# Kernel optimization log

Measured on AMD Instinct MI355X. Metric: run time of the kernel, lower is better.

## Reference

```python
import jax, jax.numpy as jnp
import numpy as np
from jax import lax

B, S, D, H = 64, 256, 512, 8
DH = D // H
FILTER_HEIGHTS = (1, 3, 5)


def setup_inputs() -> dict:
    key = jax.random.key(0)
    ks = jax.random.split(key, 20)
    w = lambda k, shape, s=0.02: (jax.random.normal(k, shape, dtype=jnp.float32) * s)
    inp = {
        "x": jax.random.normal(ks[0], (B, S, D), dtype=jnp.float32),
        "particles": jax.random.uniform(ks[1], (B, S, 3), dtype=jnp.float32),
        # QKV and output projections
        "wq": w(ks[2], (D, D)),
        "wk": w(ks[3], (D, D)),
        "wv": w(ks[4], (D, D)),
        "dense_w": w(ks[5], (D, D)),
        "dense_b": jnp.zeros((D,), jnp.float32),
        # attention-score smoothing convs: kernel (h, S, 1, 1) HWIO, full-width
        "conv1_k": w(ks[6], (1, S, 1, 1)),
        "conv1_b": jnp.zeros((1,), jnp.float32),
        "conv3_k": w(ks[7], (3, S, 1, 1)),
        "conv3_b": jnp.zeros((1,), jnp.float32),
        "conv5_k": w(ks[8], (5, S, 1, 1)),
        "conv5_b": jnp.zeros((1,), jnp.float32),
        # pairwise-feature mask net (1x1 convs == per-pair MLP): 4->8->8->1
        "mw1": w(ks[9], (4, 8), 0.1),
        "mb1": jnp.zeros((8,), jnp.float32),
        "mw2": w(ks[10], (8, 8), 0.1),
        "mb2": jnp.zeros((8,), jnp.float32),
        "mw3": w(ks[11], (8, 1), 0.1),
        "mb3": jnp.zeros((1,), jnp.float32),
    }
    return inp


def _conv_same(x, kern, bias):
    # x: [N, S, S, 1], kern: [h, S, 1, 1] -> [N, S, S, 1], TF 'same' padding, stride 1
    y = lax.conv_general_dilated(x, kern, window_strides=(1, 1), padding="SAME",
                                 dimension_numbers=("NHWC", "HWIO", "NHWC"))
    return y + bias


def _pairwise_features(particles):
    pt, eta, phi = particles[..., 0], particles[..., 1], particles[..., 2]
    pt_i, pt_j = pt[:, :, None], pt[:, None, :]
    d_eta = eta[:, :, None] - eta[:, None, :]
    dp = phi[:, :, None] - phi[:, None, :]
    d_phi = jnp.arctan2(jnp.sin(dp), jnp.cos(dp))
    delta = jnp.sqrt(d_eta ** 2 + d_phi ** 2)
    min_pt = jnp.minimum(pt_i, pt_j)
    kT = min_pt * delta
    z = min_pt / (pt_i + pt_j + 1e-8)
    m2 = jnp.maximum(pt_i ** 2 + pt_j ** 2 - 2.0 * pt_i * pt_j * jnp.cos(d_phi), 1e-8)
    eps = 1e-8
    return jnp.stack([
        jnp.log(jnp.maximum(delta, eps)),
        jnp.log(jnp.maximum(kT, eps)),
        jnp.log(jnp.maximum(z, eps)),
        jnp.log(m2),
    ], axis=-1)  # [B, S, S, 4]


def reference(x, particles, wq, wk, wv, dense_w, dense_b,
              conv1_k, conv1_b, conv3_k, conv3_b, conv5_k, conv5_b,
              mw1, mb1, mw2, mb2, mw3, mb3):
    b = x.shape[0]
    split = lambda t: t.reshape(b, S, H, DH).transpose(0, 2, 1, 3)  # [B,H,S,DH]
    q, k, v = split(x @ wq), split(x @ wk), split(x @ wv)

    scores = jnp.einsum("bhqd,bhkd->bhqk", q, k) / jnp.sqrt(jnp.float32(DH))

    # conv smoothing over score matrices (avg of full-width convs h in {1,3,5})
    xs = scores.reshape(b * H, S, S, 1)
    c1 = _conv_same(xs, conv1_k, conv1_b)
    c3 = _conv_same(xs, conv3_k, conv3_b)
    c5 = _conv_same(xs, conv5_k, conv5_b)
    scores = ((c1 + c3 + c5) / 3.0).reshape(b, H, S, S)

    # pairwise-feature mask (1x1 conv net == per-pair MLP)
    feats = _pairwise_features(particles)               # [B,S,S,4]
    m = jax.nn.relu(feats @ mw1 + mb1)
    m = jax.nn.relu(m @ mw2 + mb2)
    m = (m @ mw3 + mb3)[..., 0]                         # [B,S,S]
    m = jnp.clip(m, -10.0, 10.0)
    scores = scores + m[:, None, :, :]

    weights = jax.nn.softmax(scores, axis=-1)
    attn = jnp.einsum("bhqk,bhkd->bhqd", weights, v)
    concat = attn.transpose(0, 2, 1, 3).reshape(b, S, D)
    return concat @ dense_w + dense_b
```

## Files before the change

kernel.cpp:

```cpp
#include <hip/hip_runtime.h>
#include <hip/hip_bf16.h>
#include <math.h>

#define B   64
#define S   256
#define DD  512
#define H   8
#define DH  64
#define BH  (B*H)

typedef short s16x8 __attribute__((ext_vector_type(8)));
typedef short s16x4 __attribute__((ext_vector_type(4)));
typedef float f32x4 __attribute__((ext_vector_type(4)));

typedef __attribute__((address_space(3))) unsigned int       lds_u32;
typedef __attribute__((address_space(1))) const unsigned int glb_u32;

__device__ __forceinline__ short f2bf(float f) {
    union { float f; unsigned u; } v; v.f = f;
    unsigned u = v.u;
    u += 0x7FFFu + ((u >> 16) & 1u);
    return (short)(u >> 16);
}

__device__ __forceinline__ void glds16(const void* g, void* l) {
    __builtin_amdgcn_global_load_lds((glb_u32*)g, (lds_u32*)l, 16, 0, 0);
}

__global__ __launch_bounds__(256) void convert_x_kernel(
    const float* __restrict__ x, ushort* __restrict__ xbf)
{
    const int idx = blockIdx.x * 256 + threadIdx.x;
    const float4 f0 = *(const float4*)(x + (size_t)idx * 8);
    const float4 f1 = *(const float4*)(x + (size_t)idx * 8 + 4);
    s16x8 o = { f2bf(f0.x), f2bf(f0.y), f2bf(f0.z), f2bf(f0.w),
                f2bf(f1.x), f2bf(f1.y), f2bf(f1.z), f2bf(f1.w) };
    *(s16x8*)(xbf + (size_t)idx * 8) = o;
}

__global__ __launch_bounds__(256) void transpose_w_kernel(
    const float* __restrict__ wq, const float* __restrict__ wk,
    const float* __restrict__ wv, const float* __restrict__ wd,
    ushort* __restrict__ wt)
{
    __shared__ float tile[32][33];
    const int z = blockIdx.z;
    const float* w = (z == 0) ? wq : (z == 1) ? wk : (z == 2) ? wv : wd;
    const int k0 = blockIdx.y * 32, n0 = blockIdx.x * 32;
    const int tx = threadIdx.x & 31, ty = threadIdx.x >> 5;

    #pragma unroll
    for (int r = 0; r < 32; r += 8)
        tile[ty + r][tx] = w[(size_t)(k0 + ty + r) * DD + n0 + tx];
    __syncthreads();
    #pragma unroll
    for (int r = 0; r < 32; r += 8)
        wt[(size_t)z * DD * DD + (size_t)(n0 + ty + r) * DD + k0 + tx] =
            (ushort)f2bf(tile[tx][ty + r]);
}

__global__ __launch_bounds__(256) void build_toeplitz_frag_kernel(
    const float* __restrict__ c1k, const float* __restrict__ c3k,
    const float* __restrict__ c5k, ushort* __restrict__ btf)
{
    const int idx  = blockIdx.x * 256 + threadIdx.x;
    const int lane = idx & 63;
    const int st   = (idx >> 6) % 40;
    const int n    = idx / (40 * 64);
    const int c    = n * 16 + (lane & 15);
    const int r    = st >> 3;
    const int tb   = (st & 7) * 32 + (lane >> 4) * 8;

    s16x8 o;
    #pragma unroll
    for (int e = 0; e < 8; ++e) {
        const int ki = tb + e - c + 127;
        float val = 0.f;
        if (ki >= 0 && ki < 256) {
            val = c5k[r * 256 + ki];
            if (r >= 1 && r <= 3) val += c3k[(r - 1) * 256 + ki];
            if (r == 2)           val += c1k[ki];
            val *= (1.f / 24.f);
        }
        o[e] = f2bf(val);
    }
    *(s16x8*)(btf + (size_t)idx * 8) = o;
}

__global__ __launch_bounds__(256) void vfrag_repack_kernel(
    const ushort* __restrict__ vbT, ushort* __restrict__ vfrag)
{
    const int idx  = blockIdx.x * 256 + threadIdx.x;
    const int lane = idx & 63;
    const int kk   = (idx >> 6) & 7;
    const int n    = (idx >> 9) & 3;
    const int head = idx >> 11;
    const s16x8 v = *(const s16x8*)(vbT
        + ((size_t)(head * 64 + n * 16 + (lane & 15))) * 256
        + kk * 32 + (lane >> 4) * 8);
    *(s16x8*)(vfrag + (size_t)idx * 8) = v;
}

template<int MODE>
__global__ __launch_bounds__(256) void gemm_mfma_kernel(
    const ushort* __restrict__ A, const ushort* __restrict__ BtAll,
    ushort* __restrict__ qo, ushort* __restrict__ ko, ushort* __restrict__ vo,
    const float* __restrict__ bias, float* __restrict__ outf)
{
    __shared__ ushort As[128 * 64];
    __shared__ ushort Bs[128 * 64];

    const int tid  = threadIdx.x;
    const int lane = tid & 63, w = tid >> 6;
    const int l15  = lane & 15, l4 = lane >> 4;
    const int wr   = w >> 1, wc = w & 1;
    const int row0 = blockIdx.y * 128, col0 = blockIdx.x * 128;
    const ushort* Bt = BtAll + (MODE == 0 ? (size_t)blockIdx.z * DD * DD : 0);

    f32x4 acc[4][4];
    #pragma unroll
    for (int mt = 0; mt < 4; ++mt)
        #pragma unroll
        for (int nt = 0; nt < 4; ++nt)
            acc[mt][nt] = (f32x4){0.f, 0.f, 0.f, 0.f};

    const int arow = tid >> 3;
    const int acol = (tid & 7) * 8;
    char* ldsA = (char*)As + (tid >> 6) * 1024;
    char* ldsB = (char*)Bs + (tid >> 6) * 1024;

    for (int k0 = 0; k0 < DD; k0 += 64) {
        #pragma unroll
        for (int i = 0; i < 4; ++i)
            glds16(A  + (size_t)(row0 + arow + 32 * i) * DD + k0 + acol,
                   ldsA + 4096 * i);
        #pragma unroll
        for (int i = 0; i < 4; ++i)
            glds16(Bt + (size_t)(col0 + arow + 32 * i) * DD + k0 + acol,
                   ldsB + 4096 * i);
        __syncthreads();

        #pragma unroll
        for (int kk = 0; kk < 2; ++kk) {
            s16x8 af[4], bf[4];
            #pragma unroll
            for (int mt = 0; mt < 4; ++mt) {
                const int row = wr * 64 + mt * 16 + l15;
                af[mt] = *(const s16x8*)((char*)As + row * 128 + kk * 64 + l4 * 16);
            }
            #pragma unroll
            for (int nt = 0; nt < 4; ++nt) {
                const int col = wc * 64 + nt * 16 + l15;
                bf[nt] = *(const s16x8*)((char*)Bs + col * 128 + kk * 64 + l4 * 16);
            }
            #pragma unroll
            for (int mt = 0; mt < 4; ++mt)
                #pragma unroll
                for (int nt = 0; nt < 4; ++nt)
                    acc[mt][nt] = __builtin_amdgcn_mfma_f32_16x16x32_bf16(
                                      af[mt], bf[nt], acc[mt][nt], 0, 0, 0);
        }
        __syncthreads();
    }

    if (MODE == 0) {
        if (blockIdx.z == 2) {
            #pragma unroll
            for (int mt = 0; mt < 4; ++mt)
                #pragma unroll
                for (int nt = 0; nt < 4; ++nt) {
                    const int r = row0 + wr * 64 + mt * 16 + l4 * 4;
                    const int c = col0 + wc * 64 + nt * 16 + l15;
                    const int bb = r >> 8, ss = r & 255;
                    const int hh = c >> 6, dd = c & 63;
                    s16x4 pk = { f2bf(acc[mt][nt][0]), f2bf(acc[mt][nt][1]),
                                 f2bf(acc[mt][nt][2]), f2bf(acc[mt][nt][3]) };
                    *(s16x4*)(vo + ((size_t)((bb * H + hh) * DH + dd)) * S + ss) = pk;
                }
        } else {
            ushort* dst = (blockIdx.z == 0) ? qo : ko;
            #pragma unroll
            for (int mt = 0; mt < 4; ++mt)
                #pragma unroll
                for (int nt = 0; nt < 4; ++nt)
                    #pragma unroll
                    for (int rg = 0; rg < 4; ++rg) {
                        const int r = row0 + wr * 64 + mt * 16 + l4 * 4 + rg;
                        const int c = col0 + wc * 64 + nt * 16 + l15;
                        const int bb = r >> 8, ss = r & 255;
                        const int hh = c >> 6, dd = c & 63;
                        dst[(((size_t)(bb * H + hh)) * S + ss) * DH + dd] =
                            (ushort)f2bf(acc[mt][nt][rg]);
                    }
        }
    } else {
        #pragma unroll
        for (int mt = 0; mt < 4; ++mt)
            #pragma unroll
            for (int nt = 0; nt < 4; ++nt)
                #pragma unroll
                for (int rg = 0; rg < 4; ++rg) {
                    const int r = row0 + wr * 64 + mt * 16 + l4 * 4 + rg;
                    const int c = col0 + wc * 64 + nt * 16 + l15;
                    outf[(size_t)r * DD + c] = acc[mt][nt][rg] + bias[c];
                }
    }
}

__global__ __launch_bounds__(256) void pairwise_mlp_kernel(
    const float* __restrict__ particles,
    const float* __restrict__ mw1, const float* __restrict__ mb1,
    const float* __restrict__ mw2, const float* __restrict__ mb2,
    const float* __restrict__ mw3, const float* __restrict__ mb3,
    const float* __restrict__ c1b, const float* __restrict__ c3b,
    const float* __restrict__ c5b,
    float* __restrict__ mfrag)
{
    __shared__ float w1[32], b1[8], w2[64], b2[8], w3[8];
    __shared__ float b3s;
    const int tid = threadIdx.x;
    if (tid < 32)                 w1[tid]        = mw1[tid];
    if (tid >= 32 && tid < 40)    b1[tid - 32]   = mb1[tid - 32];
    if (tid >= 64 && tid < 128)   w2[tid - 64]   = mw2[tid - 64];
    if (tid >= 128 && tid < 136)  b2[tid - 128]  = mb2[tid - 128];
    if (tid >= 136 && tid < 144)  w3[tid - 136]  = mw3[tid - 136];
    if (tid == 144)               b3s            = mb3[0];

    const int bi = blockIdx.x;
    const int bb = bi >> 8;
    const float pt_i  = particles[(size_t)bi * 3 + 0];
    const float eta_i = particles[(size_t)bi * 3 + 1];
    const float phi_i = particles[(size_t)bi * 3 + 2];

    const int j = tid;
    const float* pj = particles + ((size_t)(bb * S) + j) * 3;
    const float pt_j = pj[0], eta_j = pj[1], phi_j = pj[2];

    __syncthreads();

    const float d_eta = eta_i - eta_j;
    const float dp    = phi_i - phi_j;
    const float d_phi = atan2f(sinf(dp), cosf(dp));
    const float delta = sqrtf(d_eta * d_eta + d_phi * d_phi);
    const float min_pt = fminf(pt_i, pt_j);
    const float kT = min_pt * delta;
    const float zf = min_pt / (pt_i + pt_j + 1e-8f);
    const float cd = cosf(d_phi);
    const float m2 = fmaxf(pt_i * pt_i + pt_j * pt_j - 2.0f * pt_i * pt_j * cd, 1e-8f);

    const float eps = 1e-8f;
    const float f[4] = { logf(fmaxf(delta, eps)),
                         logf(fmaxf(kT,    eps)),
                         logf(fmaxf(zf,    eps)),
                         logf(m2) };

    float h1[8];
    #pragma unroll
    for (int o = 0; o < 8; ++o) {
        float s = b1[o];
        #pragma unroll
        for (int i4 = 0; i4 < 4; ++i4) s += f[i4] * w1[i4 * 8 + o];
        h1[o] = fmaxf(s, 0.0f);
    }
    float h2[8];
    #pragma unroll
    for (int o = 0; o < 8; ++o) {
        float s = b2[o];
        #pragma unroll
        for (int i8 = 0; i8 < 8; ++i8) s += h1[i8] * w2[i8 * 8 + o];
        h2[o] = fmaxf(s, 0.0f);
    }
    float mv = b3s;
    #pragma unroll
    for (int i8 = 0; i8 < 8; ++i8) mv += h2[i8] * w3[i8];
    mv = fminf(fmaxf(mv, -10.0f), 10.0f);
    mv += (c1b[0] + c3b[0] + c5b[0]) * (1.f / 3.f);

    const int ii     = bi & 255;
    const int chunk2 = ii >> 7;
    const int rem    = ii & 127;
    const int wr     = rem >> 6, rt = (rem >> 4) & 3, l4h = (rem >> 2) & 3, rg = rem & 3;
    const int wc     = j >> 6,   n2 = (j >> 4) & 3,  l15 = j & 15;
    const int lane   = l4h * 16 + l15;
    const int w8     = wr * 4 + wc;
    mfrag[((((size_t)(bb * 2 + chunk2)) * 8 + w8) * 64 + lane) * 64
          + rt * 16 + n2 * 4 + rg] = mv;
}

__global__ __launch_bounds__(512, 4) void fused_mfma_kernel(
    const ushort* __restrict__ q, const ushort* __restrict__ kbuf,
    const ushort* __restrict__ vfrag, const ushort* __restrict__ btf,
    const float* __restrict__ mfrag, ushort* __restrict__ attn)
{
    __shared__ __align__(16) char pool[75776];
    char* SC   = pool;
    char* PB   = pool;
    float* RED = (float*)(pool + 73728);

    const int tid  = threadIdx.x;
    const int lane = tid & 63;
    const int w    = tid >> 6;
    const int wr   = w >> 2, wc = w & 3;
    const int l15  = lane & 15, l4 = lane >> 4;
    const int head = blockIdx.y;
    const int bb   = head >> 3, hh = head & 7;
    const int i0   = blockIdx.x * 128;
    const int cb   = wc * 64;

    {
        const ushort* kb_h = kbuf + (size_t)head * S * DH;
        const ushort* qb_h = q    + (size_t)head * S * DH;
        const int ntiles = 5 - wr;
        const int tg0    = wr * 5;
        f32x4 sacc[4][5];
        #pragma unroll
        for (int mt = 0; mt < 4; ++mt)
            #pragma unroll
            for (int nt = 0; nt < 5; ++nt)
                sacc[mt][nt] = (f32x4){0.f, 0.f, 0.f, 0.f};

        #pragma unroll
        for (int kk = 0; kk < 2; ++kk) {
            s16x8 afr[4];
            #pragma unroll
            for (int mt = 0; mt < 4; ++mt)
                afr[mt] = *(const s16x8*)(kb_h
                          + (size_t)(cb + mt * 16 + l15) * 64 + kk * 32 + 8 * l4);
            #pragma unroll
            for (int nt = 0; nt < 5; ++nt) {
                if (nt < ntiles) {
                    const int qrow = i0 - 8 + (tg0 + nt) * 16 + l15;
                    s16x8 bfr = (s16x8){0,0,0,0,0,0,0,0};
                    if ((unsigned)qrow < (unsigned)S)
                        bfr = *(const s16x8*)(qb_h + (size_t)qrow * 64 + kk * 32 + 8 * l4);
                    #pragma unroll
                    for (int mt = 0; mt < 4; ++mt)
                        sacc[mt][nt] = __builtin_amdgcn_mfma_f32_16x16x32_bf16(
                                           afr[mt], bfr, sacc[mt][nt], 0, 0, 0);
                }
            }
        }
        #pragma unroll
        for (int mt = 0; mt < 4; ++mt)
            #pragma unroll
            for (int nt = 0; nt < 5; ++nt) {
                if (nt < ntiles) {
                    const int row = (tg0 + nt) * 16 + l15;
                    const int t0  = cb + mt * 16 + l4 * 4;
                    s16x4 pk = { f2bf(sacc[mt][nt][0]), f2bf(sacc[mt][nt][1]),
                                 f2bf(sacc[mt][nt][2]), f2bf(sacc[mt][nt][3]) };
                    const int byt = (row * 512 + t0 * 2) ^ ((row & 7) << 4);
                    *(s16x4*)(SC + byt) = pk;
                }
            }
    }
    __syncthreads();

    f32x4 cacc[4][4];
    #pragma unroll
    for (int rt = 0; rt < 4; ++rt)
        #pragma unroll
        for (int n = 0; n < 4; ++n)
            cacc[rt][n] = (f32x4){0.f, 0.f, 0.f, 0.f};

    {
        const ushort* btw = btf + (size_t)(wc * 4) * 40 * 512 + lane * 8;

        s16x8 pb[2][4];
        auto ldB = [&](int st, int slot) {
            #pragma unroll
            for (int i = 0; i < 4; ++i)
                pb[slot][i] = *(const s16x8*)(btw + (size_t)(i * 40 + st) * 512);
        };
        auto convStep = [&](int st, int slot) {
            const int r = st >> 3, kb2 = (st & 7) * 64 + 16 * l4;
            #pragma unroll
            for (int rt = 0; rt < 4; ++rt) {
                const int sr = wr * 64 + rt * 16 + l15 + r + 6;
                const s16x8 afr = *(const s16x8*)(SC + ((sr * 512 + kb2) ^ ((sr & 7) << 4)));
                #pragma unroll
                for (int n = 0; n < 4; ++n)
                    cacc[rt][n] = __builtin_amdgcn_mfma_f32_16x16x32_bf16(
                                      afr, pb[slot][n], cacc[rt][n], 0, 0, 0);
            }
        };

        ldB(0, 0);
        for (int qq = 0; qq < 20; ++qq) {
            const int st = qq * 2;
            ldB(st + 1, 1);
            convStep(st + 0, 0);
            if (st + 2 < 40) ldB(st + 2, 0);
            convStep(st + 1, 1);
        }
    }

    {
        const float* mf = mfrag
            + ((((size_t)(bb * 2 + blockIdx.x)) * 8 + w) * 64 + lane) * 64;
        #pragma unroll
        for (int rt = 0; rt < 4; ++rt)
            #pragma unroll
            for (int n = 0; n < 4; ++n) {
                const float4 mv = *(const float4*)(mf + rt * 16 + n * 4);
                cacc[rt][n][0] += mv.x;
                cacc[rt][n][1] += mv.y;
                cacc[rt][n][2] += mv.z;
                cacc[rt][n][3] += mv.w;
            }
    }

    float rmax[4][4];
    #pragma unroll
    for (int rt = 0; rt < 4; ++rt)
        #pragma unroll
        for (int rg = 0; rg < 4; ++rg) {
            float mx = fmaxf(fmaxf(cacc[rt][0][rg], cacc[rt][1][rg]),
                             fmaxf(cacc[rt][2][rg], cacc[rt][3][rg]));
            mx = fmaxf(mx, __shfl_xor(mx, 1));
            mx = fmaxf(mx, __shfl_xor(mx, 2));
            mx = fmaxf(mx, __shfl_xor(mx, 4));
            mx = fmaxf(mx, __shfl_xor(mx, 8));
            rmax[rt][rg] = mx;
        }
    if (l15 == 0) {
        #pragma unroll
        for (int rt = 0; rt < 4; ++rt)
            #pragma unroll
            for (int rg = 0; rg < 4; ++rg)
                RED[(wr * 64 + rt * 16 + l4 * 4 + rg) * 4 + wc] = rmax[rt][rg];
    }
    __syncthreads();
    #pragma unroll
    for (int rt = 0; rt < 4; ++rt)
        #pragma unroll
        for (int rg = 0; rg < 4; ++rg) {
            const int row = wr * 64 + rt * 16 + l4 * 4 + rg;
            rmax[rt][rg] = fmaxf(fmaxf(RED[row * 4 + 0], RED[row * 4 + 1]),
                                 fmaxf(RED[row * 4 + 2], RED[row * 4 + 3]));
        }
    __syncthreads();

    float rinv[4][4];
    #pragma unroll
    for (int rt = 0; rt < 4; ++rt)
        #pragma unroll
        for (int rg = 0; rg < 4; ++rg) {
            float sm = 0.f;
            #pragma unroll
            for (int n = 0; n < 4; ++n) {
                const float e = __expf(cacc[rt][n][rg] - rmax[rt][rg]);
                cacc[rt][n][rg] = e;
                sm += e;
            }
            sm += __shfl_xor(sm, 1);
            sm += __shfl_xor(sm, 2);
            sm += __shfl_xor(sm, 4);
            sm += __shfl_xor(sm, 8);
            rinv[rt][rg] = sm;
        }
    if (l15 == 0) {
        #pragma unroll
        for (int rt = 0; rt < 4; ++rt)
            #pragma unroll
            for (int rg = 0; rg < 4; ++rg)
                RED[(wr * 64 + rt * 16 + l4 * 4 + rg) * 4 + wc] = rinv[rt][rg];
    }
    __syncthreads();
    #pragma unroll
    for (int rt = 0; rt < 4; ++rt)
        #pragma unroll
        for (int rg = 0; rg < 4; ++rg) {
            const int row = wr * 64 + rt * 16 + l4 * 4 + rg;
            const float tot = (RED[row * 4 + 0] + RED[row * 4 + 1])
                            + (RED[row * 4 + 2] + RED[row * 4 + 3]);
            rinv[rt][rg] = 1.f / tot;
        }
    __syncthreads();

    #pragma unroll
    for (int rt = 0; rt < 4; ++rt)
        #pragma unroll
        for (int n = 0; n < 4; ++n)
            #pragma unroll
            for (int rg = 0; rg < 4; ++rg) {
                const int row = wr * 64 + rt * 16 + l4 * 4 + rg;
                const int col = cb + n * 16 + l15;
                const int byt = (row * 512 + col * 2) ^ ((row & 7) << 4);
                *(short*)(PB + byt) = f2bf(cacc[rt][n][rg] * rinv[rt][rg]);
            }
    __syncthreads();

    const ushort* vf_h = vfrag + (size_t)head * 4 * 8 * 512 + lane * 8;
    f32x4 pacc[4];
    #pragma unroll
    for (int n = 0; n < 4; ++n) pacc[n] = (f32x4){0.f, 0.f, 0.f, 0.f};
    #pragma unroll
    for (int kk = 0; kk < 8; ++kk) {
        const int prow = w * 16 + l15;
        const int byta = (prow * 512 + kk * 64 + 16 * l4) ^ ((prow & 7) << 4);
        const s16x8 pa = *(const s16x8*)(PB + byta);
        #pragma unroll
        for (int n = 0; n < 4; ++n) {
            const s16x8 vb8 = *(const s16x8*)(vf_h + (size_t)(n * 8 + kk) * 512);
            pacc[n] = __builtin_amdgcn_mfma_f32_16x16x32_bf16(pa, vb8, pacc[n], 0, 0, 0);
        }
    }
    #pragma unroll
    for (int n = 0; n < 4; ++n)
        #pragma unroll
        for (int rg = 0; rg < 4; ++rg) {
            const int i = i0 + w * 16 + l4 * 4 + rg;
            const int d = n * 16 + l15;
            attn[(((size_t)bb * S + i) * H + hh) * DH + d] = (ushort)f2bf(pacc[n][rg]);
        }
}

extern "C" void kernel_launch(void* const* d_in, const int* in_sizes, int n_in,
                              void* d_out, int out_size, void* d_ws, size_t ws_size,
                              hipStream_t stream)
{
    (void)in_sizes; (void)n_in; (void)out_size; (void)ws_size;

    const float* x        = (const float*)d_in[0];
    const float* particles= (const float*)d_in[1];
    const float* wq       = (const float*)d_in[2];
    const float* wk       = (const float*)d_in[3];
    const float* wv       = (const float*)d_in[4];
    const float* dense_w  = (const float*)d_in[5];
    const float* dense_b  = (const float*)d_in[6];
    const float* c1k      = (const float*)d_in[7];
    const float* c1b      = (const float*)d_in[8];
    const float* c3k      = (const float*)d_in[9];
    const float* c3b      = (const float*)d_in[10];
    const float* c5k      = (const float*)d_in[11];
    const float* c5b      = (const float*)d_in[12];
    const float* mw1      = (const float*)d_in[13];
    const float* mb1      = (const float*)d_in[14];
    const float* mw2      = (const float*)d_in[15];
    const float* mb2      = (const float*)d_in[16];
    const float* mw3      = (const float*)d_in[17];
    const float* mb3      = (const float*)d_in[18];
    float* out = (float*)d_out;

    ushort* xbf   = (ushort*)d_ws;
    ushort* wt    = xbf   + (size_t)8388608;
    ushort* qb    = wt    + (size_t)1048576;
    ushort* kb    = qb    + (size_t)8388608;
    ushort* vbT   = kb    + (size_t)8388608;
    ushort* attnb = vbT   + (size_t)8388608;
    ushort* btf   = attnb + (size_t)8388608;
    ushort* vfrag = btf   + (size_t)327680;
    float*  mfrag = (float*)(vfrag + (size_t)8388608);

    convert_x_kernel<<<dim3(4096), 256, 0, stream>>>(x, xbf);
    transpose_w_kernel<<<dim3(16, 16, 4), 256, 0, stream>>>(wq, wk, wv, dense_w, wt);
    build_toeplitz_frag_kernel<<<dim3(160), 256, 0, stream>>>(c1k, c3k, c5k, btf);
    pairwise_mlp_kernel<<<dim3(B * S), 256, 0, stream>>>(
        particles, mw1, mb1, mw2, mb2, mw3, mb3, c1b, c3b, c5b, mfrag);

    gemm_mfma_kernel<0><<<dim3(4, 128, 3), 256, 0, stream>>>(
        xbf, wt, qb, kb, vbT, nullptr, nullptr);
    vfrag_repack_kernel<<<dim3(4096), 256, 0, stream>>>(vbT, vfrag);

    fused_mfma_kernel<<<dim3(2, BH), 512, 0, stream>>>(
        qb, kb, vfrag, btf, mfrag, attnb);

    gemm_mfma_kernel<1><<<dim3(4, 128, 1), 256, 0, stream>>>(
        attnb, wt + (size_t)3 * DD * DD, nullptr, nullptr, nullptr, dense_b, out);
}
```

Baseline: 278.7 us.

## Swap GEMM operand roles for vectorized Q/K and output stores, simplify phi wrap

Splits the QKV GEMM in two. Q/K and the dense projection now use a swapped-operand kernel (weights as A, tokens as B), so each lane's accumulator holds four consecutive output features and can be written with one packed bf16x4 or float4 store instead of scalar stores. V keeps the transposed layout in its own kernel. It also replaces atan2(sin,cos) phi wrapping with an rint-based modulo and uses the native bf16 conversion. The rint-based wrap can differ from atan2 at the ±pi boundary, and the bf16 cast may round slightly differently.

```diff
diff --git a/kernel.cpp b/kernel.cpp
--- a/kernel.cpp
+++ b/kernel.cpp
@@ -17,10 +17,9 @@
 typedef __attribute__((address_space(1))) const unsigned int glb_u32;
 
 __device__ __forceinline__ short f2bf(float f) {
-    union { float f; unsigned u; } v; v.f = f;
-    unsigned u = v.u;
-    u += 0x7FFFu + ((u >> 16) & 1u);
-    return (short)(u >> 16);
+    __bf16 h = (__bf16)f;
+    union { __bf16 b; short s; } u; u.b = h;
+    return u.s;
 }
 
 __device__ __forceinline__ void glds16(const void* g, void* l) {
@@ -101,11 +100,9 @@
     *(s16x8*)(vfrag + (size_t)idx * 8) = v;
 }
 
-template<int MODE>
-__global__ __launch_bounds__(256) void gemm_mfma_kernel(
-    const ushort* __restrict__ A, const ushort* __restrict__ BtAll,
-    ushort* __restrict__ qo, ushort* __restrict__ ko, ushort* __restrict__ vo,
-    const float* __restrict__ bias, float* __restrict__ outf)
+__global__ __launch_bounds__(256) void gemm_vT_kernel(
+    const ushort* __restrict__ A, const ushort* __restrict__ Bt,
+    ushort* __restrict__ vo)
 {
     __shared__ ushort As[128 * 64];
     __shared__ ushort Bs[128 * 64];
@@ -115,7 +112,6 @@
     const int l15  = lane & 15, l4 = lane >> 4;
     const int wr   = w >> 1, wc = w & 1;
     const int row0 = blockIdx.y * 128, col0 = blockIdx.x * 128;
-    const ushort* Bt = BtAll + (MODE == 0 ? (size_t)blockIdx.z * DD * DD : 0);
 
     f32x4 acc[4][4];
     #pragma unroll
@@ -163,47 +159,110 @@
         __syncthreads();
     }
 
-    if (MODE == 0) {
-        if (blockIdx.z == 2) {
-            #pragma unroll
-            for (int mt = 0; mt < 4; ++mt)
-                #pragma unroll
-                for (int nt = 0; nt < 4; ++nt) {
-                    const int r = row0 + wr * 64 + mt * 16 + l4 * 4;
-                    const int c = col0 + wc * 64 + nt * 16 + l15;
-                    const int bb = r >> 8, ss = r & 255;
-                    const int hh = c >> 6, dd = c & 63;
-                    s16x4 pk = { f2bf(acc[mt][nt][0]), f2bf(acc[mt][nt][1]),
-                                 f2bf(acc[mt][nt][2]), f2bf(acc[mt][nt][3]) };
-                    *(s16x4*)(vo + ((size_t)((bb * H + hh) * DH + dd)) * S + ss) = pk;
-                }
-        } else {
-            ushort* dst = (blockIdx.z == 0) ? qo : ko;
+    #pragma unroll
+    for (int mt = 0; mt < 4; ++mt)
+        #pragma unroll
+        for (int nt = 0; nt < 4; ++nt) {
+            const int r = row0 + wr * 64 + mt * 16 + l4 * 4;
+            const int c = col0 + wc * 64 + nt * 16 + l15;
+            const int bb = r >> 8, ss = r & 255;
+            const int hh = c >> 6, dd = c & 63;
+            s16x4 pk = { f2bf(acc[mt][nt][0]), f2bf(acc[mt][nt][1]),
+                         f2bf(acc[mt][nt][2]), f2bf(acc[mt][nt][3]) };
+            *(s16x4*)(vo + ((size_t)((bb * H + hh) * DH + dd)) * S + ss) = pk;
+        }
+}
+
+template<int MODE>
+__global__ __launch_bounds__(256) void gemm_swapped_kernel(
+    const ushort* __restrict__ WtAll, const ushort* __restrict__ Tok,
+    ushort* __restrict__ qo, ushort* __restrict__ ko,
+    const float* __restrict__ bias, float* __restrict__ outf)
+{
+    __shared__ ushort As[128 * 64];
+    __shared__ ushort Bs[128 * 64];
+
+    const int tid  = threadIdx.x;
+    const int lane = tid & 63, w = tid >> 6;
+    const int l15  = lane & 15, l4 = lane >> 4;
+    const int wr   = w >> 1, wc = w & 1;
+    const int frow0 = blockIdx.y * 128;
+    const int trow0 = blockIdx.x * 128;
+    const ushort* A = WtAll + (MODE == 0 ? (size_t)blockIdx.z * DD * DD : 0);
+
+    f32x4 acc[4][4];
+    #pragma unroll
+    for (int mt = 0; mt < 4; ++mt)
+        #pragma unroll
+        for (int nt = 0; nt < 4; ++nt)
+            acc[mt][nt] = (f32x4){0.f, 0.f, 0.f, 0.f};
+
+    const int arow = tid >> 3;
+    const int acol = (tid & 7) * 8;
+    char* ldsA = (char*)As + (tid >> 6) * 1024;
+    char* ldsB = (char*)Bs + (tid >> 6) * 1024;
+
+    for (int k0 = 0; k0 < DD; k0 += 64) {
+        #pragma unroll
+        for (int i = 0; i < 4; ++i)
+            glds16(A   + (size_t)(frow0 + arow + 32 * i) * DD + k0 + acol,
+                   ldsA + 4096 * i);
+        #pragma unroll
+        for (int i = 0; i < 4; ++i)
+            glds16(Tok + (size_t)(trow0 + arow + 32 * i) * DD + k0 + acol,
+                   ldsB + 4096 * i);
+        __syncthreads();
+
+        #pragma unroll
+        for (int kk = 0; kk < 2; ++kk) {
+            s16x8 af[4], bf[4];
+            #pragma unroll
+            for (int mt = 0; mt < 4; ++mt) {
+                const int row = wr * 64 + mt * 16 + l15;
+                af[mt] = *(const s16x8*)((char*)As + row * 128 + kk * 64 + l4 * 16);
+            }
+            #pragma unroll
+            for (int nt = 0; nt < 4; ++nt) {
+                const int col = wc * 64 + nt * 16 + l15;
+                bf[nt] = *(const s16x8*)((char*)Bs + col * 128 + kk * 64 + l4 * 16);
+            }
             #pragma unroll
             for (int mt = 0; mt < 4; ++mt)
                 #pragma unroll
                 for (int nt = 0; nt < 4; ++nt)
-                    #pragma unroll
-                    for (int rg = 0; rg < 4; ++rg) {
-                        const int r = row0 + wr * 64 + mt * 16 + l4 * 4 + rg;
-                        const int c = col0 + wc * 64 + nt * 16 + l15;
-                        const int bb = r >> 8, ss = r & 255;
-                        const int hh = c >> 6, dd = c & 63;
-                        dst[(((size_t)(bb * H + hh)) * S + ss) * DH + dd] =
-                            (ushort)f2bf(acc[mt][nt][rg]);
-                    }
-        }
+                    acc[mt][nt] = __builtin_amdgcn_mfma_f32_16x16x32_bf16(
+                                      af[mt], bf[nt], acc[mt][nt], 0, 0, 0);
+        }
+        __syncthreads();
+    }
+
+    if (MODE == 0) {
+        ushort* dst = (blockIdx.z == 0) ? qo : ko;
+        #pragma unroll
+        for (int mt = 0; mt < 4; ++mt)
+            #pragma unroll
+            for (int nt = 0; nt < 4; ++nt) {
+                const int r = trow0 + wc * 64 + nt * 16 + l15;
+                const int c = frow0 + wr * 64 + mt * 16 + l4 * 4;
+                const int bb = r >> 8, ss = r & 255;
+                const int hh = c >> 6, dd = c & 63;
+                s16x4 pk = { f2bf(acc[mt][nt][0]), f2bf(acc[mt][nt][1]),
+                             f2bf(acc[mt][nt][2]), f2bf(acc[mt][nt][3]) };
+                *(s16x4*)(dst + (((size_t)(bb * H + hh)) * S + ss) * DH + dd) = pk;
+            }
     } else {
         #pragma unroll
-        for (int mt = 0; mt < 4; ++mt)
-            #pragma unroll
-            for (int nt = 0; nt < 4; ++nt)
-                #pragma unroll
-                for (int rg = 0; rg < 4; ++rg) {
-                    const int r = row0 + wr * 64 + mt * 16 + l4 * 4 + rg;
-                    const int c = col0 + wc * 64 + nt * 16 + l15;
-                    outf[(size_t)r * DD + c] = acc[mt][nt][rg] + bias[c];
-                }
+        for (int mt = 0; mt < 4; ++mt) {
+            const int c = frow0 + wr * 64 + mt * 16 + l4 * 4;
+            const float4 b4 = *(const float4*)(bias + c);
+            #pragma unroll
+            for (int nt = 0; nt < 4; ++nt) {
+                const int r = trow0 + wc * 64 + nt * 16 + l15;
+                float4 o = make_float4(acc[mt][nt][0] + b4.x, acc[mt][nt][1] + b4.y,
+                                       acc[mt][nt][2] + b4.z, acc[mt][nt][3] + b4.w);
+                *(float4*)(outf + (size_t)r * DD + c) = o;
+            }
+        }
     }
 }
 
@@ -240,7 +299,8 @@
 
     const float d_eta = eta_i - eta_j;
     const float dp    = phi_i - phi_j;
-    const float d_phi = atan2f(sinf(dp), cosf(dp));
+    const float d_phi = dp - 6.28318530717958647692f
+                             * rintf(dp * 0.15915494309189533577f);
     const float delta = sqrtf(d_eta * d_eta + d_phi * d_phi);
     const float min_pt = fminf(pt_i, pt_j);
     const float kT = min_pt * delta;
@@ -559,13 +619,15 @@
     pairwise_mlp_kernel<<<dim3(B * S), 256, 0, stream>>>(
         particles, mw1, mb1, mw2, mb2, mw3, mb3, c1b, c3b, c5b, mfrag);
 
-    gemm_mfma_kernel<0><<<dim3(4, 128, 3), 256, 0, stream>>>(
-        xbf, wt, qb, kb, vbT, nullptr, nullptr);
+    gemm_swapped_kernel<0><<<dim3(128, 4, 2), 256, 0, stream>>>(
+        wt, xbf, qb, kb, nullptr, nullptr);
+    gemm_vT_kernel<<<dim3(4, 128), 256, 0, stream>>>(
+        xbf, wt + (size_t)2 * DD * DD, vbT);
     vfrag_repack_kernel<<<dim3(4096), 256, 0, stream>>>(vbT, vfrag);
 
     fused_mfma_kernel<<<dim3(2, BH), 512, 0, stream>>>(
         qb, kb, vfrag, btf, mfrag, attnb);
 
-    gemm_mfma_kernel<1><<<dim3(4, 128, 1), 256, 0, stream>>>(
-        attnb, wt + (size_t)3 * DD * DD, nullptr, nullptr, nullptr, dense_b, out);
-}
+    gemm_swapped_kernel<1><<<dim3(128, 4), 256, 0, stream>>>(
+        wt + (size_t)3 * DD * DD, attnb, nullptr, nullptr, dense_b, out);
+}
```

Result: no change. 276.7 us (-0.7%).
